# Optimization experiments

Measured on AMD Instinct MI355X. Metric: run time of the kernel, lower is better.

Reference implementation:

```python
import jax, jax.numpy as jnp
import numpy as np

N_NODES = 100000
N_EDGES = 1600000
D_FEAT = 64
HIDDEN = 64


def _glorot(key, shape):
    fan_in, fan_out = shape[1], shape[0]
    limit = float(np.sqrt(6.0 / (fan_in + fan_out)))
    return jax.random.uniform(key, shape, jnp.float32, -limit, limit)


def setup_inputs() -> dict:
    key = jax.random.key(0)
    ks = jax.random.split(key, 8)
    x = jax.random.normal(ks[0], (N_NODES, D_FEAT), jnp.float32)
    edge_index = jax.random.randint(ks[1], (2, N_EDGES), 0, N_NODES, jnp.int64)
    # SAGEConv params: lin_l applied to aggregated neighbors (has bias),
    # lin_r applied to root/self features (no bias in PyG default).
    params = {
        "W1_l": _glorot(ks[2], (HIDDEN, D_FEAT)),
        "b1": jnp.zeros((HIDDEN,), jnp.float32),
        "W1_r": _glorot(ks[3], (HIDDEN, D_FEAT)),
        "W2_l": _glorot(ks[4], (HIDDEN, HIDDEN)),
        "b2": jnp.zeros((HIDDEN,), jnp.float32),
        "W2_r": _glorot(ks[5], (HIDDEN, HIDDEN)),
    }
    return {"x": x, "edge_index": edge_index, **params}


def _sage_conv(x, src, dst, deg_inv, W_l, b, W_r):
    # mean-aggregate neighbor features: gather at src, segment-sum at dst
    msg = jax.ops.segment_sum(x[src], dst, num_segments=N_NODES)  # [N, F]
    agg = msg * deg_inv[:, None]
    return agg @ W_l.T + b + x @ W_r.T


def reference(x, edge_index, W1_l, b1, W1_r, W2_l, b2, W2_r):
    src, dst = edge_index[0], edge_index[1]
    deg = jax.ops.segment_sum(jnp.ones((N_EDGES,), x.dtype), dst,
                              num_segments=N_NODES)
    deg_inv = 1.0 / jnp.maximum(deg, 1.0)  # PyG mean clamps count to >=1
    h = jax.nn.relu(_sage_conv(x, src, dst, deg_inv, W1_l, b1, W1_r))
    out = _sage_conv(h, src, dst, deg_inv, W2_l, b2, W2_r)
    return out
```

## Files before the change

kernel.cpp:

```cpp
#include <hip/hip_runtime.h>
#include <hip/hip_bf16.h>

#define FEAT 64

typedef __bf16 bf16x8 __attribute__((ext_vector_type(8)));
typedef __bf16 bf16x4 __attribute__((ext_vector_type(4)));
typedef float  f32x4  __attribute__((ext_vector_type(4)));

__global__ __launch_bounds__(256)
void zero2_kernel(int* __restrict__ a, int* __restrict__ b, int n) {
    int i = blockIdx.x * 256 + threadIdx.x;
    if (i < n) { a[i] = 0; b[i] = 0; }
}

__global__ void detect_idx_kernel(const unsigned* __restrict__ w, int* __restrict__ flag,
                                  int* __restrict__ zcnt) {
    __shared__ int any_nz;
    if (threadIdx.x == 0) any_nz = 0;
    __syncthreads();
    if (w[2 * threadIdx.x + 1] != 0u) atomicOr(&any_nz, 1);
    zcnt[threadIdx.x] = 0;
    zcnt[threadIdx.x + 256] = 0;
    __syncthreads();
    if (threadIdx.x == 0) *flag = (any_nz == 0) ? 1 : 0;
}

__device__ __forceinline__ int load_idx_clamped(const void* ei, long long i, int is64, int n_nodes) {
    int v = is64 ? ((const int*)ei)[2 * i] : ((const int*)ei)[i];
    v = v < 0 ? 0 : v;
    return v >= n_nodes ? n_nodes - 1 : v;
}


__global__ __launch_bounds__(256)
void bucket_count_kernel(const void* __restrict__ ei, const int* __restrict__ flagp,
                         int* __restrict__ gcnt, int n_edges, int n_nodes) {
    __shared__ int cnt[512];
    const int t = threadIdx.x;
    cnt[t] = 0; cnt[t + 256] = 0;
    __syncthreads();
    const int is64 = *flagp;
    for (int e = blockIdx.x * 256 + t; e < n_edges; e += gridDim.x * 256) {
        int d = load_idx_clamped(ei, (long long)n_edges + e, is64, n_nodes);
        atomicAdd(&cnt[d >> 9], 1);
    }
    __syncthreads();
    if (cnt[t])       atomicAdd(&gcnt[t], cnt[t]);
    if (cnt[t + 256]) atomicAdd(&gcnt[t + 256], cnt[t + 256]);
}

__global__ void bucket_scan_kernel(const int* __restrict__ gcnt, int* __restrict__ gbase,
                                   int* __restrict__ gcur, int n_edges) {
    __shared__ int sh[512];
    int t = threadIdx.x;
    int v = gcnt[t];
    sh[t] = v;
    __syncthreads();
    for (int off = 1; off < 512; off <<= 1) {
        int u = (t >= off) ? sh[t - off] : 0;
        __syncthreads();
        sh[t] += u;
        __syncthreads();
    }
    int excl = sh[t] - v;
    gbase[t] = excl;
    gcur[t]  = excl;
    if (t == 511) gbase[512] = n_edges;
}

__global__ __launch_bounds__(256)
void multisplit_kernel(const void* __restrict__ ei, const int* __restrict__ flagp,
                       int* __restrict__ gcur, unsigned* __restrict__ B,
                       int n_edges, int n_nodes) {
    __shared__ unsigned sv[4096];
    __shared__ unsigned dv[4096];
    __shared__ int cnt[512];
    __shared__ int cur[512];
    const int t = threadIdx.x;
    const int is64 = *flagp;
    const int ntiles = (n_edges + 4095) >> 12;
    for (int tile = blockIdx.x; tile < ntiles; tile += gridDim.x) {
        cnt[t] = 0; cnt[t + 256] = 0;
        __syncthreads();
        #pragma unroll
        for (int k = 0; k < 16; ++k) {
            int i = k * 256 + t;
            int e = (tile << 12) + i;
            unsigned dmark = 0xFFFFFFFFu, s = 0;
            if (e < n_edges) {
                s     = (unsigned)load_idx_clamped(ei, e, is64, n_nodes);
                int d = load_idx_clamped(ei, (long long)n_edges + e, is64, n_nodes);
                dmark = (unsigned)d;
                atomicAdd(&cnt[d >> 9], 1);
            }
            sv[i] = s; dv[i] = dmark;
        }
        __syncthreads();
        if (cnt[t])       cur[t]       = atomicAdd(&gcur[t], cnt[t]);
        if (cnt[t + 256]) cur[t + 256] = atomicAdd(&gcur[t + 256], cnt[t + 256]);
        __syncthreads();
        #pragma unroll
        for (int k = 0; k < 16; ++k) {
            int i = k * 256 + t;
            unsigned d = dv[i];
            if (d != 0xFFFFFFFFu) {
                int pos = atomicAdd(&cur[d >> 9], 1);
                pos = pos < 0 ? 0 : (pos >= n_edges ? n_edges - 1 : pos);
                B[pos] = ((d & 511u) << 17) | sv[i];
            }
        }
        __syncthreads();
    }
}

__global__ __launch_bounds__(256)
void csr_build2_kernel(const unsigned* __restrict__ B, const int* __restrict__ gbase,
                       int* __restrict__ degc, int* __restrict__ offs,
                       float* __restrict__ dinv, int* __restrict__ csr,
                       int n_edges, int n_nodes) {
    __shared__ int cnt[512];
    __shared__ int scn[512];
    __shared__ int cur[512];
    const int b = blockIdx.x, t = threadIdx.x;
    cnt[t] = 0; cnt[t + 256] = 0;
    __syncthreads();
    const int lo = gbase[b], hi = gbase[b + 1];
    for (int i = lo + t; i < hi; i += 256) {
        unsigned v = B[i];
        atomicAdd(&cnt[v >> 17], 1);
    }
    __syncthreads();
    scn[t] = cnt[t]; scn[t + 256] = cnt[t + 256];
    __syncthreads();
    for (int off = 1; off < 512; off <<= 1) {
        int u0 = (t >= off) ? scn[t - off] : 0;
        int u1 = (t + 256 >= off) ? scn[t + 256 - off] : 0;
        __syncthreads();
        scn[t] += u0; scn[t + 256] += u1;
        __syncthreads();
    }
    const int base = gbase[b];
    int e0 = base + scn[t] - cnt[t];
    int e1 = base + scn[t + 256] - cnt[t + 256];
    cur[t] = e0; cur[t + 256] = e1;
    int n0 = b * 512 + t, n1 = n0 + 256;
    if (n0 < n_nodes) {
        degc[n0] = cnt[t]; offs[n0] = e0;
        dinv[n0] = 1.0f / fmaxf((float)cnt[t], 1.0f);
    }
    if (n1 < n_nodes) {
        degc[n1] = cnt[t + 256]; offs[n1] = e1;
        dinv[n1] = 1.0f / fmaxf((float)cnt[t + 256], 1.0f);
    }
    __syncthreads();
    for (int i = lo + t; i < hi; i += 256) {
        unsigned v = B[i];
        int pos = atomicAdd(&cur[v >> 17], 1);
        pos = pos < 0 ? 0 : (pos >= n_edges ? n_edges - 1 : pos);
        csr[pos] = (int)(v & 0x1FFFFu);
    }
}

__global__ __launch_bounds__(256)
void scan_partial_kernel(const int* __restrict__ degc, int* __restrict__ part, int n_nodes) {
    __shared__ int sh[256];
    int i = blockIdx.x * 256 + threadIdx.x;
    sh[threadIdx.x] = (i < n_nodes) ? degc[i] : 0;
    __syncthreads();
    for (int off = 128; off > 0; off >>= 1) {
        if (threadIdx.x < off) sh[threadIdx.x] += sh[threadIdx.x + off];
        __syncthreads();
    }
    if (threadIdx.x == 0) part[blockIdx.x] = sh[0];
}

__global__ void scan_top_kernel(int* __restrict__ part, int nparts) {
    __shared__ int sh[512];
    int t = threadIdx.x;
    int v = (t < nparts) ? part[t] : 0;
    sh[t] = v;
    __syncthreads();
    for (int off = 1; off < 512; off <<= 1) {
        int u = (t >= off) ? sh[t - off] : 0;
        __syncthreads();
        sh[t] += u;
        __syncthreads();
    }
    if (t < nparts) part[t] = sh[t] - v;
}

__global__ __launch_bounds__(256)
void scan_final_kernel(const int* __restrict__ degc, const int* __restrict__ part,
                       int* __restrict__ offs, float* __restrict__ deg_inv, int n_nodes) {
    __shared__ int sh[256];
    int t = threadIdx.x;
    int i = blockIdx.x * 256 + t;
    int v = (i < n_nodes) ? degc[i] : 0;
    sh[t] = v;
    __syncthreads();
    for (int off = 1; off < 256; off <<= 1) {
        int u = (t >= off) ? sh[t - off] : 0;
        __syncthreads();
        sh[t] += u;
        __syncthreads();
    }
    if (i < n_nodes) {
        offs[i]    = sh[t] - v + part[blockIdx.x];
        deg_inv[i] = 1.0f / fmaxf((float)v, 1.0f);
    }
}

__global__ __launch_bounds__(256)
void hist_kernel(const void* __restrict__ ei, const int* __restrict__ flagp,
                 int* __restrict__ degc, int n_edges, int n_nodes) {
    int e = blockIdx.x * 256 + threadIdx.x;
    if (e >= n_edges) return;
    int d = load_idx_clamped(ei, (long long)n_edges + e, *flagp, n_nodes);
    atomicAdd(&degc[d], 1);
}

__global__ __launch_bounds__(256)
void csr_scatter_kernel(const void* __restrict__ ei, const int* __restrict__ flagp,
                        const int* __restrict__ offs, int* __restrict__ cursor,
                        int* __restrict__ csr, int n_edges, int n_nodes) {
    int e = blockIdx.x * 256 + threadIdx.x;
    if (e >= n_edges) return;
    int is64 = *flagp;
    int s = load_idx_clamped(ei, e, is64, n_nodes);
    int d = load_idx_clamped(ei, (long long)n_edges + e, is64, n_nodes);
    int pos = offs[d] + atomicAdd(&cursor[d], 1);
    pos = pos < 0 ? 0 : (pos >= n_edges ? n_edges - 1 : pos);
    csr[pos] = s;
}

__global__ __launch_bounds__(256)
void cast_w_kernel(const float* __restrict__ a, const float* __restrict__ b,
                   const float* __restrict__ c, const float* __restrict__ d,
                   __bf16* __restrict__ o) {
    int i = blockIdx.x * 256 + threadIdx.x;
    if (i < FEAT * FEAT) {
        o[i]         = (__bf16)a[i];
        o[4096 + i]  = (__bf16)b[i];
        o[8192 + i]  = (__bf16)c[i];
        o[12288 + i] = (__bf16)d[i];
    }
}

__global__ __launch_bounds__(256)
void cast_x_kernel(const float* __restrict__ x, __bf16* __restrict__ xb, int n4) {
    int i = blockIdx.x * 256 + threadIdx.x;
    if (i < n4) {
        float4 v = ((const float4*)x)[i];
        bf16x4 o;
        o.x = (__bf16)v.x; o.y = (__bf16)v.y; o.z = (__bf16)v.z; o.w = (__bf16)v.w;
        ((bf16x4*)xb)[i] = o;
    }
}

__global__ __launch_bounds__(256)
void gather_bf16_kernel(const __bf16* __restrict__ hin, const int* __restrict__ offs,
                        const int* __restrict__ degc, const float* __restrict__ dinv,
                        const int* __restrict__ csr, __bf16* __restrict__ agg,
                        int n_nodes) {
    const int t = threadIdx.x, u = t & 15;
    const int g0 = blockIdx.x * 16 + (t >> 4);
    const int ng = gridDim.x * 16;
    if (g0 >= n_nodes) return;
    int rs = offs[g0], cnt = degc[g0];
    float di = dinv[g0];
    int idx = (u < cnt) ? (int)__builtin_nontemporal_load(&csr[rs + u]) : 0;
    for (int n = g0; n < n_nodes; n += ng) {
        const int nn = n + ng;
        int rs2 = 0, cnt2 = 0;
        float di2 = 1.0f;
        if (nn < n_nodes) { rs2 = offs[nn]; cnt2 = degc[nn]; di2 = dinv[nn]; }
        float a0 = 0.f, a1 = 0.f, a2 = 0.f, a3 = 0.f;
        int c = 0;
        while (true) {
            idx = idx < 0 ? 0 : (idx >= n_nodes ? n_nodes - 1 : idx);
            int sj[16];
            #pragma unroll
            for (int j = 0; j < 16; ++j) sj[j] = __shfl(idx, j, 16);
            bf16x4 v[16];
            #pragma unroll
            for (int j = 0; j < 16; ++j)
                v[j] = ((const bf16x4*)hin)[(size_t)sj[j] * 16 + u];
            #pragma unroll
            for (int j = 0; j < 16; ++j) {
                float m = (c + j < cnt) ? 1.f : 0.f;
                a0 = fmaf(m, (float)v[j].x, a0);
                a1 = fmaf(m, (float)v[j].y, a1);
                a2 = fmaf(m, (float)v[j].z, a2);
                a3 = fmaf(m, (float)v[j].w, a3);
            }
            c += 16;
            if (c >= cnt) break;
            idx = (u < cnt - c) ? (int)__builtin_nontemporal_load(&csr[rs + c + u]) : 0;
        }
        idx = (nn < n_nodes && u < cnt2)
                  ? (int)__builtin_nontemporal_load(&csr[rs2 + u]) : 0;
        bf16x4 o;
        o.x = (__bf16)(a0 * di); o.y = (__bf16)(a1 * di);
        o.z = (__bf16)(a2 * di); o.w = (__bf16)(a3 * di);
        ((bf16x4*)agg)[(size_t)n * 16 + u] = o;
        rs = rs2; cnt = cnt2; di = di2;
    }
}

__global__ __launch_bounds__(256)
void gather_f32_kernel(const float* __restrict__ xin, const int* __restrict__ offs,
                       const int* __restrict__ degc, const float* __restrict__ dinv,
                       const int* __restrict__ csr, __bf16* __restrict__ agg,
                       int n_nodes) {
    const int t = threadIdx.x, lane = t & 63, g = lane >> 4, u = lane & 15;
    const int gw = blockIdx.x * 4 + (t >> 6), nw = gridDim.x * 4;
    for (int n = gw; n < n_nodes; n += nw) {
        int rs = offs[n], cnt = degc[n];
        float a0 = 0.f, a1 = 0.f, a2 = 0.f, a3 = 0.f;
        for (int c = 0; c < cnt; c += 64) {
            int chunk = min(64, cnt - c);
            int myid = (lane < chunk) ? (int)__builtin_nontemporal_load(&csr[rs + c + lane]) : 0;
            myid = myid < 0 ? 0 : (myid >= n_nodes ? n_nodes - 1 : myid);
            for (int q = 0; q < chunk; q += 16) {
                int q0 = q + g, q1 = q + g + 4, q2 = q + g + 8, q3 = q + g + 12;
                int s0 = __shfl(myid, q0), s1 = __shfl(myid, q1);
                int s2 = __shfl(myid, q2), s3 = __shfl(myid, q3);
                float m0 = (q0 < chunk) ? 1.f : 0.f;
                float m1 = (q1 < chunk) ? 1.f : 0.f;
                float m2 = (q2 < chunk) ? 1.f : 0.f;
                float m3 = (q3 < chunk) ? 1.f : 0.f;
                float4 v0 = ((const float4*)xin)[(size_t)s0 * 16 + u];
                float4 v1 = ((const float4*)xin)[(size_t)s1 * 16 + u];
                float4 v2 = ((const float4*)xin)[(size_t)s2 * 16 + u];
                float4 v3 = ((const float4*)xin)[(size_t)s3 * 16 + u];
                a0 = fmaf(m0, v0.x, a0); a1 = fmaf(m0, v0.y, a1);
                a2 = fmaf(m0, v0.z, a2); a3 = fmaf(m0, v0.w, a3);
                a0 = fmaf(m1, v1.x, a0); a1 = fmaf(m1, v1.y, a1);
                a2 = fmaf(m1, v1.z, a2); a3 = fmaf(m1, v1.w, a3);
                a0 = fmaf(m2, v2.x, a0); a1 = fmaf(m2, v2.y, a1);
                a2 = fmaf(m2, v2.z, a2); a3 = fmaf(m2, v2.w, a3);
                a0 = fmaf(m3, v3.x, a0); a1 = fmaf(m3, v3.y, a1);
                a2 = fmaf(m3, v3.z, a2); a3 = fmaf(m3, v3.w, a3);
            }
        }
        a0 += __shfl_xor(a0, 16); a1 += __shfl_xor(a1, 16);
        a2 += __shfl_xor(a2, 16); a3 += __shfl_xor(a3, 16);
        a0 += __shfl_xor(a0, 32); a1 += __shfl_xor(a1, 32);
        a2 += __shfl_xor(a2, 32); a3 += __shfl_xor(a3, 32);
        if (g == 0) {
            float di = dinv[n];
            bf16x4 o;
            o.x = (__bf16)(a0 * di); o.y = (__bf16)(a1 * di);
            o.z = (__bf16)(a2 * di); o.w = (__bf16)(a3 * di);
            ((bf16x4*)agg)[(size_t)n * 16 + u] = o;
        }
    }
}

__global__ __launch_bounds__(256)
void gemm_l1b_kernel(const __bf16* __restrict__ Ag, const __bf16* __restrict__ xb,
                     const __bf16* __restrict__ Bl, const __bf16* __restrict__ Br,
                     const float* __restrict__ bias,
                     __bf16* __restrict__ hout, int n_nodes) {
    const int t = threadIdx.x, lane = t & 63;
    const int quad = lane >> 4, r16 = lane & 15;
    bf16x8 bl[2][4], br[2][4];
    #pragma unroll
    for (int ks = 0; ks < 2; ++ks)
        #pragma unroll
        for (int ct = 0; ct < 4; ++ct) {
            int f = ct * 16 + r16, k = ks * 32 + quad * 8;
            bl[ks][ct] = *(const bf16x8*)(Bl + f * 64 + k);
            br[ks][ct] = *(const bf16x8*)(Br + f * 64 + k);
        }
    const int m0 = (blockIdx.x * 4 + (t >> 6)) * 16;
    if (m0 >= n_nodes) return;
    int mrow = m0 + r16; if (mrow >= n_nodes) mrow = n_nodes - 1;
    bf16x8 ag[2], ax[2];
    #pragma unroll
    for (int ks = 0; ks < 2; ++ks) {
        ag[ks] = *(const bf16x8*)(Ag + (size_t)mrow * 64 + ks * 32 + quad * 8);
        ax[ks] = *(const bf16x8*)(xb + (size_t)mrow * 64 + ks * 32 + quad * 8);
    }
    #pragma unroll
    for (int ct = 0; ct < 4; ++ct) {
        f32x4 acc = {0.f, 0.f, 0.f, 0.f};
        acc = __builtin_amdgcn_mfma_f32_16x16x32_bf16(ag[0], bl[0][ct], acc, 0, 0, 0);
        acc = __builtin_amdgcn_mfma_f32_16x16x32_bf16(ag[1], bl[1][ct], acc, 0, 0, 0);
        acc = __builtin_amdgcn_mfma_f32_16x16x32_bf16(ax[0], br[0][ct], acc, 0, 0, 0);
        acc = __builtin_amdgcn_mfma_f32_16x16x32_bf16(ax[1], br[1][ct], acc, 0, 0, 0);
        int col = ct * 16 + r16;
        float bv = bias[col];
        #pragma unroll
        for (int rg = 0; rg < 4; ++rg) {
            int n = m0 + quad * 4 + rg;
            if (n < n_nodes) {
                float o = acc[rg] + bv;
                hout[(size_t)n * 64 + col] = (__bf16)fmaxf(o, 0.f);
            }
        }
    }
}

__global__ __launch_bounds__(256)
void gemm_l1_kernel(const __bf16* __restrict__ Ag, const float* __restrict__ xin,
                    const __bf16* __restrict__ Bl, const __bf16* __restrict__ Br,
                    const float* __restrict__ bias,
                    __bf16* __restrict__ hout, int n_nodes) {
    const int t = threadIdx.x, lane = t & 63;
    const int quad = lane >> 4, r16 = lane & 15;
    bf16x8 bl[2][4], br[2][4];
    #pragma unroll
    for (int ks = 0; ks < 2; ++ks)
        #pragma unroll
        for (int ct = 0; ct < 4; ++ct) {
            int f = ct * 16 + r16, k = ks * 32 + quad * 8;
            bl[ks][ct] = *(const bf16x8*)(Bl + f * 64 + k);
            br[ks][ct] = *(const bf16x8*)(Br + f * 64 + k);
        }
    const int m0 = (blockIdx.x * 4 + (t >> 6)) * 16;
    if (m0 >= n_nodes) return;
    int mrow = m0 + r16; if (mrow >= n_nodes) mrow = n_nodes - 1;
    bf16x8 ag[2], ax[2];
    #pragma unroll
    for (int ks = 0; ks < 2; ++ks) {
        ag[ks] = *(const bf16x8*)(Ag + (size_t)mrow * 64 + ks * 32 + quad * 8);
        const float* xr = xin + (size_t)mrow * 64 + ks * 32 + quad * 8;
        float4 p = *(const float4*)xr;
        float4 q = *(const float4*)(xr + 4);
        union { bf16x8 v; __bf16 e[8]; } U;
        U.e[0] = (__bf16)p.x; U.e[1] = (__bf16)p.y; U.e[2] = (__bf16)p.z; U.e[3] = (__bf16)p.w;
        U.e[4] = (__bf16)q.x; U.e[5] = (__bf16)q.y; U.e[6] = (__bf16)q.z; U.e[7] = (__bf16)q.w;
        ax[ks] = U.v;
    }
    #pragma unroll
    for (int ct = 0; ct < 4; ++ct) {
        f32x4 acc = {0.f, 0.f, 0.f, 0.f};
        acc = __builtin_amdgcn_mfma_f32_16x16x32_bf16(ag[0], bl[0][ct], acc, 0, 0, 0);
        acc = __builtin_amdgcn_mfma_f32_16x16x32_bf16(ag[1], bl[1][ct], acc, 0, 0, 0);
        acc = __builtin_amdgcn_mfma_f32_16x16x32_bf16(ax[0], br[0][ct], acc, 0, 0, 0);
        acc = __builtin_amdgcn_mfma_f32_16x16x32_bf16(ax[1], br[1][ct], acc, 0, 0, 0);
        int col = ct * 16 + r16;
        float bv = bias[col];
        #pragma unroll
        for (int rg = 0; rg < 4; ++rg) {
            int n = m0 + quad * 4 + rg;
            if (n < n_nodes) {
                float o = acc[rg] + bv;
                hout[(size_t)n * 64 + col] = (__bf16)fmaxf(o, 0.f);
            }
        }
    }
}

__global__ __launch_bounds__(256)
void gemm_l2_kernel(const __bf16* __restrict__ Ag, const __bf16* __restrict__ Ah,
                    const __bf16* __restrict__ Bl, const __bf16* __restrict__ Br,
                    const float* __restrict__ bias,
                    float* __restrict__ out, int n_nodes) {
    const int t = threadIdx.x, lane = t & 63;
    const int quad = lane >> 4, r16 = lane & 15;
    bf16x8 bl[2][4], br[2][4];
    #pragma unroll
    for (int ks = 0; ks < 2; ++ks)
        #pragma unroll
        for (int ct = 0; ct < 4; ++ct) {
            int f = ct * 16 + r16, k = ks * 32 + quad * 8;
            bl[ks][ct] = *(const bf16x8*)(Bl + f * 64 + k);
            br[ks][ct] = *(const bf16x8*)(Br + f * 64 + k);
        }
    const int m0 = (blockIdx.x * 4 + (t >> 6)) * 16;
    if (m0 >= n_nodes) return;
    int mrow = m0 + r16; if (mrow >= n_nodes) mrow = n_nodes - 1;
    bf16x8 ag[2], ah[2];
    #pragma unroll
    for (int ks = 0; ks < 2; ++ks) {
        ag[ks] = *(const bf16x8*)(Ag + (size_t)mrow * 64 + ks * 32 + quad * 8);
        ah[ks] = *(const bf16x8*)(Ah + (size_t)mrow * 64 + ks * 32 + quad * 8);
    }
    #pragma unroll
    for (int ct = 0; ct < 4; ++ct) {
        f32x4 acc = {0.f, 0.f, 0.f, 0.f};
        acc = __builtin_amdgcn_mfma_f32_16x16x32_bf16(ag[0], bl[0][ct], acc, 0, 0, 0);
        acc = __builtin_amdgcn_mfma_f32_16x16x32_bf16(ag[1], bl[1][ct], acc, 0, 0, 0);
        acc = __builtin_amdgcn_mfma_f32_16x16x32_bf16(ah[0], br[0][ct], acc, 0, 0, 0);
        acc = __builtin_amdgcn_mfma_f32_16x16x32_bf16(ah[1], br[1][ct], acc, 0, 0, 0);
        int col = ct * 16 + r16;
        float bv = bias[col];
        #pragma unroll
        for (int rg = 0; rg < 4; ++rg) {
            int n = m0 + quad * 4 + rg;
            if (n < n_nodes) out[(size_t)n * 64 + col] = acc[rg] + bv;
        }
    }
}

__global__ __launch_bounds__(256)
void sage_fused_l1_kernel(const float* __restrict__ xin,
                          const int* __restrict__ offs, const int* __restrict__ degc,
                          const float* __restrict__ deg_inv, const int* __restrict__ csr,
                          const float* __restrict__ Wl, const float* __restrict__ bias,
                          const float* __restrict__ Wr,
                          __bf16* __restrict__ hout, int n_nodes) {
    __shared__ float WlT[FEAT * 65], WrT[FEAT * 65], bsh[FEAT];
    __shared__ float aggS[4][FEAT], selfS[4][FEAT];
    const int t = threadIdx.x;
    #pragma unroll
    for (int p = 0; p < 16; ++p) {
        int i = t + p * 256, j = i >> 6, k = i & 63;
        WlT[k * 65 + j] = Wl[i];
        WrT[k * 65 + j] = Wr[i];
    }
    if (t < FEAT) bsh[t] = bias[t];
    __syncthreads();
    const int w = t >> 6, f = t & 63;
    const int n_groups = (n_nodes + 3) >> 2;
    for (int g = blockIdx.x; g < n_groups; g += gridDim.x) {
        int n = g * 4 + w;
        bool act = (n < n_nodes);
        if (act) {
            int rs = offs[n], cnt = degc[n];
            float acc = 0.f;
            for (int c = 0; c < cnt; c += 64) {
                int chunk = min(64, cnt - c);
                int myid = (f < chunk) ? csr[rs + c + f] : 0;
                #pragma unroll 4
                for (int q = 0; q < chunk; ++q) {
                    int s = __shfl(myid, q);
                    acc += xin[(long long)s * FEAT + f];
                }
            }
            aggS[w][f]  = acc * deg_inv[n];
            selfS[w][f] = xin[(long long)n * FEAT + f];
        }
        __syncthreads();
        if (act) {
            float o = bsh[f];
            #pragma unroll
            for (int k = 0; k < FEAT; ++k) {
                o = fmaf(aggS[w][k],  WlT[k * 65 + f], o);
                o = fmaf(selfS[w][k], WrT[k * 65 + f], o);
            }
            o = fmaxf(o, 0.f);
            hout[(long long)n * FEAT + f] = (__bf16)o;
        }
        __syncthreads();
    }
}

__global__ __launch_bounds__(256)
void sage_fused_l2_kernel(const __bf16* __restrict__ hin,
                          const int* __restrict__ offs, const int* __restrict__ degc,
                          const float* __restrict__ deg_inv, const int* __restrict__ csr,
                          const float* __restrict__ Wl, const float* __restrict__ bias,
                          const float* __restrict__ Wr,
                          float* __restrict__ out, int n_nodes) {
    __shared__ float WlT[FEAT * 65], WrT[FEAT * 65], bsh[FEAT];
    __shared__ float aggS[4][FEAT], selfS[4][FEAT];
    const int t = threadIdx.x;
    #pragma unroll
    for (int p = 0; p < 16; ++p) {
        int i = t + p * 256, j = i >> 6, k = i & 63;
        WlT[k * 65 + j] = Wl[i];
        WrT[k * 65 + j] = Wr[i];
    }
    if (t < FEAT) bsh[t] = bias[t];
    __syncthreads();
    const int w = t >> 6, f = t & 63;
    const int n_groups = (n_nodes + 3) >> 2;
    for (int g = blockIdx.x; g < n_groups; g += gridDim.x) {
        int n = g * 4 + w;
        bool act = (n < n_nodes);
        if (act) {
            int rs = offs[n], cnt = degc[n];
            float acc = 0.f;
            for (int c = 0; c < cnt; c += 64) {
                int chunk = min(64, cnt - c);
                int myid = (f < chunk) ? csr[rs + c + f] : 0;
                #pragma unroll 4
                for (int q = 0; q < chunk; ++q) {
                    int s = __shfl(myid, q);
                    acc += (float)hin[(long long)s * FEAT + f];
                }
            }
            aggS[w][f]  = acc * deg_inv[n];
            selfS[w][f] = (float)hin[(long long)n * FEAT + f];
        }
        __syncthreads();
        if (act) {
            float o = bsh[f];
            #pragma unroll
            for (int k = 0; k < FEAT; ++k) {
                o = fmaf(aggS[w][k],  WlT[k * 65 + f], o);
                o = fmaf(selfS[w][k], WrT[k * 65 + f], o);
            }
            out[(long long)n * FEAT + f] = o;
        }
        __syncthreads();
    }
}

extern "C" void kernel_launch(void* const* d_in, const int* in_sizes, int n_in,
                              void* d_out, int out_size, void* d_ws, size_t ws_size,
                              hipStream_t stream) {
    const float* x   = (const float*)d_in[0];
    const void*  ei  = d_in[1];
    const float* W1l = (const float*)d_in[2];
    const float* b1  = (const float*)d_in[3];
    const float* W1r = (const float*)d_in[4];
    const float* W2l = (const float*)d_in[5];
    const float* b2  = (const float*)d_in[6];
    const float* W2r = (const float*)d_in[7];
    float* out = (float*)d_out;

    const int n_nodes = in_sizes[0] / FEAT;
    const int n_edges = in_sizes[1] / 2;
    const int nparts  = (n_nodes + 255) / 256;
    const int egrid   = (n_edges + 255) / 256;
    const int NB      = (n_nodes + 511) >> 9;

    char* ws = (char*)d_ws;
    auto al = [](size_t v) { return (v + 255) & ~(size_t)255; };

    size_t o = 0;
    int*      flag  = (int*)(ws + o);      o += 256;
    int*      degc  = (int*)(ws + o);      o += al((size_t)n_nodes * 4);
    float*    dinv  = (float*)(ws + o);    o += al((size_t)n_nodes * 4);
    int*      offs  = (int*)(ws + o);      o += al((size_t)n_nodes * 4);
    int*      gcnt  = (int*)(ws + o);      o += al(512 * 4);
    int*      gbase = (int*)(ws + o);      o += al(513 * 4);
    int*      gcur  = (int*)(ws + o);      o += al(512 * 4);
    unsigned* B     = (unsigned*)(ws + o); o += al((size_t)n_edges * 4);
    int*      csr   = (int*)(ws + o);      o += al((size_t)n_edges * 4);
    __bf16*   xb    = (__bf16*)(ws + o);   o += al((size_t)n_nodes * FEAT * 2);
    __bf16*   wb    = (__bf16*)(ws + o);   o += al((size_t)4 * FEAT * FEAT * 2);
    __bf16*   agg   = (__bf16*)(ws + o);   o += al((size_t)n_nodes * FEAT * 2);
    __bf16*   h     = (__bf16*)(ws + o);   o += al((size_t)n_nodes * FEAT * 2);
    const size_t needT1 = o;

    size_t o3 = 0;
    int*    flag3   = (int*)(ws + o3);    o3 += 256;
    int*    degc3   = (int*)(ws + o3);    o3 += al((size_t)n_nodes * 4);
    float*  dinv3   = (float*)(ws + o3);  o3 += al((size_t)n_nodes * 4);
    int*    offs3   = (int*)(ws + o3);    o3 += al((size_t)n_nodes * 4);
    int*    cursor3 = (int*)(ws + o3);    o3 += al((size_t)n_nodes * 4);
    int*    part3   = (int*)(ws + o3);    o3 += al(2048);
    int*    csr3    = (int*)(ws + o3);    o3 += al((size_t)n_edges * 4);
    const size_t commonEnd3 = o3;
    __bf16* wb3  = (__bf16*)(ws + o3);    o3 += al((size_t)4 * FEAT * FEAT * 2);
    __bf16* agg3 = (__bf16*)(ws + o3);    o3 += al((size_t)n_nodes * FEAT * 2);
    __bf16* h3   = (__bf16*)(ws + o3);    o3 += al((size_t)n_nodes * FEAT * 2);
    const size_t needT3 = o3;

    const int n4 = n_nodes * FEAT / 4;
    const int mgrid = (n_nodes + 63) / 64;
    const int ggrid = 2048;
    const int ntiles = (n_edges + 4095) >> 12;

    if (ws_size >= needT1 && n_nodes <= 131072) {
        detect_idx_kernel<<<1, 256, 0, stream>>>((const unsigned*)ei, flag, gcnt);
        bucket_count_kernel<<<512, 256, 0, stream>>>(ei, flag, gcnt, n_edges, n_nodes);
        bucket_scan_kernel<<<1, 512, 0, stream>>>(gcnt, gbase, gcur, n_edges);
        multisplit_kernel<<<ntiles, 256, 0, stream>>>(ei, flag, gcur, B, n_edges, n_nodes);
        cast_x_kernel<<<(n4 + 255) / 256, 256, 0, stream>>>(x, xb, n4);
        cast_w_kernel<<<16, 256, 0, stream>>>(W1l, W1r, W2l, W2r, wb);
        csr_build2_kernel<<<NB, 256, 0, stream>>>(B, gbase, degc, offs, dinv, csr, n_edges, n_nodes);
        gather_bf16_kernel<<<ggrid, 256, 0, stream>>>(xb, offs, degc, dinv, csr, agg, n_nodes);
        gemm_l1b_kernel<<<mgrid, 256, 0, stream>>>(agg, xb, wb, wb + 4096, b1, h, n_nodes);
        gather_bf16_kernel<<<ggrid, 256, 0, stream>>>(h, offs, degc, dinv, csr, agg, n_nodes);
        gemm_l2_kernel<<<mgrid, 256, 0, stream>>>(agg, h, wb + 8192, wb + 12288, b2, out, n_nodes);
    } else if (ws_size >= needT3) {
        zero2_kernel<<<nparts, 256, 0, stream>>>(degc3, cursor3, n_nodes);
        detect_idx_kernel<<<1, 256, 0, stream>>>((const unsigned*)ei, flag3, part3);
        hist_kernel<<<egrid, 256, 0, stream>>>(ei, flag3, degc3, n_edges, n_nodes);
        scan_partial_kernel<<<nparts, 256, 0, stream>>>(degc3, part3, n_nodes);
        scan_top_kernel<<<1, 512, 0, stream>>>(part3, nparts);
        scan_final_kernel<<<nparts, 256, 0, stream>>>(degc3, part3, offs3, dinv3, n_nodes);
        csr_scatter_kernel<<<egrid, 256, 0, stream>>>(ei, flag3, offs3, cursor3, csr3, n_edges, n_nodes);
        cast_w_kernel<<<16, 256, 0, stream>>>(W1l, W1r, W2l, W2r, wb3);
        gather_f32_kernel<<<ggrid, 256, 0, stream>>>(x, offs3, degc3, dinv3, csr3, agg3, n_nodes);
        gemm_l1_kernel<<<mgrid, 256, 0, stream>>>(agg3, x, wb3, wb3 + 4096, b1, h3, n_nodes);
        gather_bf16_kernel<<<ggrid, 256, 0, stream>>>(h3, offs3, degc3, dinv3, csr3, agg3, n_nodes);
        gemm_l2_kernel<<<mgrid, 256, 0, stream>>>(agg3, h3, wb3 + 8192, wb3 + 12288, b2, out, n_nodes);
    } else {
        __bf16* hf = (__bf16*)(ws + commonEnd3);
        zero2_kernel<<<nparts, 256, 0, stream>>>(degc3, cursor3, n_nodes);
        detect_idx_kernel<<<1, 256, 0, stream>>>((const unsigned*)ei, flag3, part3);
        hist_kernel<<<egrid, 256, 0, stream>>>(ei, flag3, degc3, n_edges, n_nodes);
        scan_partial_kernel<<<nparts, 256, 0, stream>>>(degc3, part3, n_nodes);
        scan_top_kernel<<<1, 512, 0, stream>>>(part3, nparts);
        scan_final_kernel<<<nparts, 256, 0, stream>>>(degc3, part3, offs3, dinv3, n_nodes);
        csr_scatter_kernel<<<egrid, 256, 0, stream>>>(ei, flag3, offs3, cursor3, csr3, n_edges, n_nodes);
        const int n_groups = (n_nodes + 3) / 4;
        const int fgrid = n_groups < 4096 ? n_groups : 4096;
        sage_fused_l1_kernel<<<fgrid, 256, 0, stream>>>(x, offs3, degc3, dinv3, csr3,
                                                        W1l, b1, W1r, hf, n_nodes);
        sage_fused_l2_kernel<<<fgrid, 256, 0, stream>>>(hf, offs3, degc3, dinv3, csr3,
                                                        W2l, b2, W2r, out, n_nodes);
    }
}
```

Before: 267.7 us.

## Fuse neighbor gather with MFMA linear layers and merge setup kernels

Each SAGE layer's mean-aggregation gather is fused with its bf16 MFMA GEMM. A block aggregates a 16-node tile into shared memory and immediately computes that tile's output, so the aggregated tensor is never written to or re-read from global memory. The small setup kernels are also merged: index detection with the weight cast, and bucket counting with the x cast, to cut launch count. The trade-offs are a fixed 16-neighbor unrolled gather per node, which wastes loads on low-degree nodes, and two block-wide syncs per tile.

Result: faster. 240.0 us (-10.4%).

```diff
diff --git a/kernel.cpp b/kernel.cpp
--- a/kernel.cpp
+++ b/kernel.cpp
@@ -11,6 +11,31 @@
 void zero2_kernel(int* __restrict__ a, int* __restrict__ b, int n) {
     int i = blockIdx.x * 256 + threadIdx.x;
     if (i < n) { a[i] = 0; b[i] = 0; }
+}
+
+__global__ void detect_castw_kernel(const unsigned* __restrict__ w, int* __restrict__ flag,
+                                    int* __restrict__ zcnt,
+                                    const float* __restrict__ a, const float* __restrict__ b,
+                                    const float* __restrict__ c, const float* __restrict__ d,
+                                    __bf16* __restrict__ o) {
+    if (blockIdx.x == 0) {
+        __shared__ int any_nz;
+        if (threadIdx.x == 0) any_nz = 0;
+        __syncthreads();
+        if (w[2 * threadIdx.x + 1] != 0u) atomicOr(&any_nz, 1);
+        zcnt[threadIdx.x] = 0;
+        zcnt[threadIdx.x + 256] = 0;
+        __syncthreads();
+        if (threadIdx.x == 0) *flag = (any_nz == 0) ? 1 : 0;
+    } else {
+        int i = (blockIdx.x - 1) * 256 + threadIdx.x;
+        if (i < FEAT * FEAT) {
+            o[i]         = (__bf16)a[i];
+            o[4096 + i]  = (__bf16)b[i];
+            o[8192 + i]  = (__bf16)c[i];
+            o[12288 + i] = (__bf16)d[i];
+        }
+    }
 }
 
 __global__ void detect_idx_kernel(const unsigned* __restrict__ w, int* __restrict__ flag,
@@ -33,20 +58,32 @@
 
 
 __global__ __launch_bounds__(256)
-void bucket_count_kernel(const void* __restrict__ ei, const int* __restrict__ flagp,
-                         int* __restrict__ gcnt, int n_edges, int n_nodes) {
+void bucket_count_castx_kernel(const void* __restrict__ ei, const int* __restrict__ flagp,
+                               int* __restrict__ gcnt,
+                               const float* __restrict__ x, __bf16* __restrict__ xb, int n4,
+                               int n_edges, int n_nodes) {
     __shared__ int cnt[512];
     const int t = threadIdx.x;
-    cnt[t] = 0; cnt[t + 256] = 0;
-    __syncthreads();
-    const int is64 = *flagp;
-    for (int e = blockIdx.x * 256 + t; e < n_edges; e += gridDim.x * 256) {
-        int d = load_idx_clamped(ei, (long long)n_edges + e, is64, n_nodes);
-        atomicAdd(&cnt[d >> 9], 1);
-    }
-    __syncthreads();
-    if (cnt[t])       atomicAdd(&gcnt[t], cnt[t]);
-    if (cnt[t + 256]) atomicAdd(&gcnt[t + 256], cnt[t + 256]);
+    if (blockIdx.x < 512) {
+        cnt[t] = 0; cnt[t + 256] = 0;
+        __syncthreads();
+        const int is64 = *flagp;
+        for (int e = blockIdx.x * 256 + t; e < n_edges; e += 512 * 256) {
+            int d = load_idx_clamped(ei, (long long)n_edges + e, is64, n_nodes);
+            atomicAdd(&cnt[d >> 9], 1);
+        }
+        __syncthreads();
+        if (cnt[t])       atomicAdd(&gcnt[t], cnt[t]);
+        if (cnt[t + 256]) atomicAdd(&gcnt[t + 256], cnt[t + 256]);
+    } else {
+        const int nb = gridDim.x - 512;
+        for (int i = (blockIdx.x - 512) * 256 + t; i < n4; i += nb * 256) {
+            float4 v = ((const float4*)x)[i];
+            bf16x4 o;
+            o.x = (__bf16)v.x; o.y = (__bf16)v.y; o.z = (__bf16)v.z; o.w = (__bf16)v.w;
+            ((bf16x4*)xb)[i] = o;
+        }
+    }
 }
 
 __global__ void bucket_scan_kernel(const int* __restrict__ gcnt, int* __restrict__ gbase,
@@ -254,6 +291,167 @@
         bf16x4 o;
         o.x = (__bf16)v.x; o.y = (__bf16)v.y; o.z = (__bf16)v.z; o.w = (__bf16)v.w;
         ((bf16x4*)xb)[i] = o;
+    }
+}
+
+__global__ __launch_bounds__(256)
+void fused_l1_kernel(const __bf16* __restrict__ xb,
+                     const int* __restrict__ offs, const int* __restrict__ degc,
+                     const float* __restrict__ dinv, const int* __restrict__ csr,
+                     const __bf16* __restrict__ Bl, const __bf16* __restrict__ Br,
+                     const float* __restrict__ bias,
+                     __bf16* __restrict__ hout, int n_nodes) {
+    const int t = threadIdx.x, lane = t & 63, wave = t >> 6;
+    const int quad = lane >> 4, r16 = lane & 15;
+    const int grp = t >> 4, u = t & 15;
+    bf16x8 bl[2], br[2];
+    #pragma unroll
+    for (int ks = 0; ks < 2; ++ks) {
+        int f = wave * 16 + r16, k = ks * 32 + quad * 8;
+        bl[ks] = *(const bf16x8*)(Bl + f * 64 + k);
+        br[ks] = *(const bf16x8*)(Br + f * 64 + k);
+    }
+    const float bv = bias[wave * 16 + r16];
+    __shared__ __bf16 sAgg[16][72];
+    const int ntiles = (n_nodes + 15) >> 4;
+    for (int tile = blockIdx.x; tile < ntiles; tile += gridDim.x) {
+        const int n = tile * 16 + grp;
+        const bool act = n < n_nodes;
+        float a0 = 0.f, a1 = 0.f, a2 = 0.f, a3 = 0.f, di = 1.f;
+        if (act) {
+            int rs = offs[n], cnt = degc[n];
+            di = dinv[n];
+            int idx = (u < cnt) ? (int)__builtin_nontemporal_load(&csr[rs + u]) : 0;
+            int c = 0;
+            while (true) {
+                idx = idx < 0 ? 0 : (idx >= n_nodes ? n_nodes - 1 : idx);
+                int sj[16];
+                #pragma unroll
+                for (int j = 0; j < 16; ++j) sj[j] = __shfl(idx, j, 16);
+                bf16x4 v[16];
+                #pragma unroll
+                for (int j = 0; j < 16; ++j)
+                    v[j] = ((const bf16x4*)xb)[(size_t)sj[j] * 16 + u];
+                #pragma unroll
+                for (int j = 0; j < 16; ++j) {
+                    float m = (c + j < cnt) ? 1.f : 0.f;
+                    a0 = fmaf(m, (float)v[j].x, a0);
+                    a1 = fmaf(m, (float)v[j].y, a1);
+                    a2 = fmaf(m, (float)v[j].z, a2);
+                    a3 = fmaf(m, (float)v[j].w, a3);
+                }
+                c += 16;
+                if (c >= cnt) break;
+                idx = (u < cnt - c) ? (int)__builtin_nontemporal_load(&csr[rs + c + u]) : 0;
+            }
+        }
+        bf16x4 o;
+        o.x = (__bf16)(a0 * di); o.y = (__bf16)(a1 * di);
+        o.z = (__bf16)(a2 * di); o.w = (__bf16)(a3 * di);
+        *(bf16x4*)(&sAgg[grp][u * 4]) = o;
+        __syncthreads();
+        const int m0 = tile * 16;
+        int mrow = m0 + r16; if (mrow >= n_nodes) mrow = n_nodes - 1;
+        bf16x8 ag[2], ax[2];
+        #pragma unroll
+        for (int ks = 0; ks < 2; ++ks) {
+            ag[ks] = *(const bf16x8*)(&sAgg[r16][ks * 32 + quad * 8]);
+            ax[ks] = *(const bf16x8*)(xb + (size_t)mrow * 64 + ks * 32 + quad * 8);
+        }
+        f32x4 acc = {0.f, 0.f, 0.f, 0.f};
+        acc = __builtin_amdgcn_mfma_f32_16x16x32_bf16(ag[0], bl[0], acc, 0, 0, 0);
+        acc = __builtin_amdgcn_mfma_f32_16x16x32_bf16(ag[1], bl[1], acc, 0, 0, 0);
+        acc = __builtin_amdgcn_mfma_f32_16x16x32_bf16(ax[0], br[0], acc, 0, 0, 0);
+        acc = __builtin_amdgcn_mfma_f32_16x16x32_bf16(ax[1], br[1], acc, 0, 0, 0);
+        const int col = wave * 16 + r16;
+        #pragma unroll
+        for (int rg = 0; rg < 4; ++rg) {
+            int row = m0 + quad * 4 + rg;
+            if (row < n_nodes) {
+                float ov = acc[rg] + bv;
+                hout[(size_t)row * 64 + col] = (__bf16)fmaxf(ov, 0.f);
+            }
+        }
+        __syncthreads();
+    }
+}
+
+__global__ __launch_bounds__(256)
+void fused_l2_kernel(const __bf16* __restrict__ hb,
+                     const int* __restrict__ offs, const int* __restrict__ degc,
+                     const float* __restrict__ dinv, const int* __restrict__ csr,
+                     const __bf16* __restrict__ Bl, const __bf16* __restrict__ Br,
+                     const float* __restrict__ bias,
+                     float* __restrict__ out, int n_nodes) {
+    const int t = threadIdx.x, lane = t & 63, wave = t >> 6;
+    const int quad = lane >> 4, r16 = lane & 15;
+    const int grp = t >> 4, u = t & 15;
+    bf16x8 bl[2], br[2];
+    #pragma unroll
+    for (int ks = 0; ks < 2; ++ks) {
+        int f = wave * 16 + r16, k = ks * 32 + quad * 8;
+        bl[ks] = *(const bf16x8*)(Bl + f * 64 + k);
+        br[ks] = *(const bf16x8*)(Br + f * 64 + k);
+    }
+    const float bv = bias[wave * 16 + r16];
+    __shared__ __bf16 sAgg[16][72];
+    const int ntiles = (n_nodes + 15) >> 4;
+    for (int tile = blockIdx.x; tile < ntiles; tile += gridDim.x) {
+        const int n = tile * 16 + grp;
+        const bool act = n < n_nodes;
+        float a0 = 0.f, a1 = 0.f, a2 = 0.f, a3 = 0.f, di = 1.f;
+        if (act) {
+            int rs = offs[n], cnt = degc[n];
+            di = dinv[n];
+            int idx = (u < cnt) ? (int)__builtin_nontemporal_load(&csr[rs + u]) : 0;
+            int c = 0;
+            while (true) {
+                idx = idx < 0 ? 0 : (idx >= n_nodes ? n_nodes - 1 : idx);
+                int sj[16];
+                #pragma unroll
+                for (int j = 0; j < 16; ++j) sj[j] = __shfl(idx, j, 16);
+                bf16x4 v[16];
+                #pragma unroll
+                for (int j = 0; j < 16; ++j)
+                    v[j] = ((const bf16x4*)hb)[(size_t)sj[j] * 16 + u];
+                #pragma unroll
+                for (int j = 0; j < 16; ++j) {
+                    float m = (c + j < cnt) ? 1.f : 0.f;
+                    a0 = fmaf(m, (float)v[j].x, a0);
+                    a1 = fmaf(m, (float)v[j].y, a1);
+                    a2 = fmaf(m, (float)v[j].z, a2);
+                    a3 = fmaf(m, (float)v[j].w, a3);
+                }
+                c += 16;
+                if (c >= cnt) break;
+                idx = (u < cnt - c) ? (int)__builtin_nontemporal_load(&csr[rs + c + u]) : 0;
+            }
+        }
+        bf16x4 o;
+        o.x = (__bf16)(a0 * di); o.y = (__bf16)(a1 * di);
+        o.z = (__bf16)(a2 * di); o.w = (__bf16)(a3 * di);
+        *(bf16x4*)(&sAgg[grp][u * 4]) = o;
+        __syncthreads();
+        const int m0 = tile * 16;
+        int mrow = m0 + r16; if (mrow >= n_nodes) mrow = n_nodes - 1;
+        bf16x8 ag[2], ah[2];
+        #pragma unroll
+        for (int ks = 0; ks < 2; ++ks) {
+            ag[ks] = *(const bf16x8*)(&sAgg[r16][ks * 32 + quad * 8]);
+            ah[ks] = *(const bf16x8*)(hb + (size_t)mrow * 64 + ks * 32 + quad * 8);
+        }
+        f32x4 acc = {0.f, 0.f, 0.f, 0.f};
+        acc = __builtin_amdgcn_mfma_f32_16x16x32_bf16(ag[0], bl[0], acc, 0, 0, 0);
+        acc = __builtin_amdgcn_mfma_f32_16x16x32_bf16(ag[1], bl[1], acc, 0, 0, 0);
+        acc = __builtin_amdgcn_mfma_f32_16x16x32_bf16(ah[0], br[0], acc, 0, 0, 0);
+        acc = __builtin_amdgcn_mfma_f32_16x16x32_bf16(ah[1], br[1], acc, 0, 0, 0);
+        const int col = wave * 16 + r16;
+        #pragma unroll
+        for (int rg = 0; rg < 4; ++rg) {
+            int row = m0 + quad * 4 + rg;
+            if (row < n_nodes) out[(size_t)row * 64 + col] = acc[rg] + bv;
+        }
+        __syncthreads();
     }
 }
 
@@ -358,51 +556,6 @@
 }
 
 __global__ __launch_bounds__(256)
-void gemm_l1b_kernel(const __bf16* __restrict__ Ag, const __bf16* __restrict__ xb,
-                     const __bf16* __restrict__ Bl, const __bf16* __restrict__ Br,
-                     const float* __restrict__ bias,
-                     __bf16* __restrict__ hout, int n_nodes) {
-    const int t = threadIdx.x, lane = t & 63;
-    const int quad = lane >> 4, r16 = lane & 15;
-    bf16x8 bl[2][4], br[2][4];
-    #pragma unroll
-    for (int ks = 0; ks < 2; ++ks)
-        #pragma unroll
-        for (int ct = 0; ct < 4; ++ct) {
-            int f = ct * 16 + r16, k = ks * 32 + quad * 8;
-            bl[ks][ct] = *(const bf16x8*)(Bl + f * 64 + k);
-            br[ks][ct] = *(const bf16x8*)(Br + f * 64 + k);
-        }
-    const int m0 = (blockIdx.x * 4 + (t >> 6)) * 16;
-    if (m0 >= n_nodes) return;
-    int mrow = m0 + r16; if (mrow >= n_nodes) mrow = n_nodes - 1;
-    bf16x8 ag[2], ax[2];
-    #pragma unroll
-    for (int ks = 0; ks < 2; ++ks) {
-        ag[ks] = *(const bf16x8*)(Ag + (size_t)mrow * 64 + ks * 32 + quad * 8);
-        ax[ks] = *(const bf16x8*)(xb + (size_t)mrow * 64 + ks * 32 + quad * 8);
-    }
-    #pragma unroll
-    for (int ct = 0; ct < 4; ++ct) {
-        f32x4 acc = {0.f, 0.f, 0.f, 0.f};
-        acc = __builtin_amdgcn_mfma_f32_16x16x32_bf16(ag[0], bl[0][ct], acc, 0, 0, 0);
-        acc = __builtin_amdgcn_mfma_f32_16x16x32_bf16(ag[1], bl[1][ct], acc, 0, 0, 0);
-        acc = __builtin_amdgcn_mfma_f32_16x16x32_bf16(ax[0], br[0][ct], acc, 0, 0, 0);
-        acc = __builtin_amdgcn_mfma_f32_16x16x32_bf16(ax[1], br[1][ct], acc, 0, 0, 0);
-        int col = ct * 16 + r16;
-        float bv = bias[col];
-        #pragma unroll
-        for (int rg = 0; rg < 4; ++rg) {
-            int n = m0 + quad * 4 + rg;
-            if (n < n_nodes) {
-                float o = acc[rg] + bv;
-                hout[(size_t)n * 64 + col] = (__bf16)fmaxf(o, 0.f);
-            }
-        }
-    }
-}
-
-__global__ __launch_bounds__(256)
 void gemm_l1_kernel(const __bf16* __restrict__ Ag, const float* __restrict__ xin,
                     const __bf16* __restrict__ Bl, const __bf16* __restrict__ Br,
                     const float* __restrict__ bias,
@@ -634,7 +787,6 @@
     int*      csr   = (int*)(ws + o);      o += al((size_t)n_edges * 4);
     __bf16*   xb    = (__bf16*)(ws + o);   o += al((size_t)n_nodes * FEAT * 2);
     __bf16*   wb    = (__bf16*)(ws + o);   o += al((size_t)4 * FEAT * FEAT * 2);
-    __bf16*   agg   = (__bf16*)(ws + o);   o += al((size_t)n_nodes * FEAT * 2);
     __bf16*   h     = (__bf16*)(ws + o);   o += al((size_t)n_nodes * FEAT * 2);
     const size_t needT1 = o;
 
@@ -656,19 +808,21 @@
     const int mgrid = (n_nodes + 63) / 64;
     const int ggrid = 2048;
     const int ntiles = (n_edges + 4095) >> 12;
+    const int ftiles = (n_nodes + 15) >> 4;
+    const int fgrid2 = ftiles < 2048 ? ftiles : 2048;
 
     if (ws_size >= needT1 && n_nodes <= 131072) {
-        detect_idx_kernel<<<1, 256, 0, stream>>>((const unsigned*)ei, flag, gcnt);
-        bucket_count_kernel<<<512, 256, 0, stream>>>(ei, flag, gcnt, n_edges, n_nodes);
+        detect_castw_kernel<<<17, 256, 0, stream>>>((const unsigned*)ei, flag, gcnt,
+                                                    W1l, W1r, W2l, W2r, wb);
+        bucket_count_castx_kernel<<<1536, 256, 0, stream>>>(ei, flag, gcnt,
+                                                            x, xb, n4, n_edges, n_nodes);
         bucket_scan_kernel<<<1, 512, 0, stream>>>(gcnt, gbase, gcur, n_edges);
         multisplit_kernel<<<ntiles, 256, 0, stream>>>(ei, flag, gcur, B, n_edges, n_nodes);
-        cast_x_kernel<<<(n4 + 255) / 256, 256, 0, stream>>>(x, xb, n4);
-        cast_w_kernel<<<16, 256, 0, stream>>>(W1l, W1r, W2l, W2r, wb);
         csr_build2_kernel<<<NB, 256, 0, stream>>>(B, gbase, degc, offs, dinv, csr, n_edges, n_nodes);
-        gather_bf16_kernel<<<ggrid, 256, 0, stream>>>(xb, offs, degc, dinv, csr, agg, n_nodes);
-        gemm_l1b_kernel<<<mgrid, 256, 0, stream>>>(agg, xb, wb, wb + 4096, b1, h, n_nodes);
-        gather_bf16_kernel<<<ggrid, 256, 0, stream>>>(h, offs, degc, dinv, csr, agg, n_nodes);
-        gemm_l2_kernel<<<mgrid, 256, 0, stream>>>(agg, h, wb + 8192, wb + 12288, b2, out, n_nodes);
+        fused_l1_kernel<<<fgrid2, 256, 0, stream>>>(xb, offs, degc, dinv, csr,
+                                                    wb, wb + 4096, b1, h, n_nodes);
+        fused_l2_kernel<<<fgrid2, 256, 0, stream>>>(h, offs, degc, dinv, csr,
+                                                    wb + 8192, wb + 12288, b2, out, n_nodes);
     } else if (ws_size >= needT3) {
         zero2_kernel<<<nparts, 256, 0, stream>>>(degc3, cursor3, n_nodes);
         detect_idx_kernel<<<1, 256, 0, stream>>>((const unsigned*)ei, flag3, part3);
```
